# Kernel tuning notes

Measured on AMD Instinct MI355X. Metric: run time of the kernel, lower is better.

The kernel has to match this reference:

```python
import jax, jax.numpy as jnp
import numpy as np

B, T, L = 256, 2048, 48  # batch, seq_len, nb_labels


def setup_inputs() -> dict:
    key = jax.random.key(0)
    k1, k2, k3 = jax.random.split(key, 3)
    emissions = jax.random.normal(k1, (B, T, L), dtype=jnp.float32)
    tags = jax.random.randint(k2, (B, T), 0, L, dtype=jnp.int32)
    # matches nn.init.uniform_(transitions, -0.1, 0.1)
    transitions = jax.random.uniform(k3, (L, L), dtype=jnp.float32, minval=-0.1, maxval=0.1)
    return {"emissions": emissions, "tags": tags, "transitions": transitions}


def _gold_scores(emissions, tags, transitions):
    # emission score at every gold tag: [B, T] -> sum over T
    e = jnp.take_along_axis(emissions, tags[..., None], axis=2)[..., 0].sum(axis=1)
    # transition scores between consecutive gold tags
    t = transitions[tags[:, :-1], tags[:, 1:]].sum(axis=1)
    start = transitions[0, tags[:, 0]]      # row 0 acts as start scores
    end = transitions[tags[:, -1], -1]      # last column acts as end scores
    return e + t + start + end              # [B]


def _log_partition(emissions, transitions):
    # forward algorithm: alpha_t[b, j] = logsumexp_i(alpha_{t-1}[b, i] + T[i, j]) + em[b, t, j]
    alpha0 = transitions[0][None, :] + emissions[:, 0]          # [B, L]
    em_rest = jnp.moveaxis(emissions[:, 1:], 1, 0)              # [T-1, B, L]

    def step(alpha, em_t):
        alpha = jax.nn.logsumexp(alpha[:, :, None] + transitions[None, :, :], axis=1) + em_t
        return alpha, None

    alpha, _ = jax.lax.scan(step, alpha0, em_rest)
    return jax.nn.logsumexp(alpha + transitions[:, -1][None, :], axis=1)  # [B]


def reference(emissions, tags, transitions):
    """neg_log_likelihood of LinearChainCRF: -sum(scores - log_partition)."""
    scores = _gold_scores(emissions, tags, transitions)
    partition = _log_partition(emissions, transitions)
    return -jnp.sum(scores - partition)
```

## Files before the change

### kernel.cpp

```cpp
#include <hip/hip_runtime.h>

#define B 256
#define T 2048
#define L 48
#define G 16
#define SEG 128
#define KNORM 4.371f
#define TOTALF (B * T * L)

typedef short v4s __attribute__((ext_vector_type(4)));
typedef short v8s __attribute__((ext_vector_type(8)));
typedef float v4f __attribute__((ext_vector_type(4)));
typedef int   v2i __attribute__((ext_vector_type(2)));

#define WAVE_SYNC() asm volatile("s_waitcnt lgkmcnt(0)" ::: "memory")

#if __has_builtin(__builtin_amdgcn_mfma_f32_16x16x16bf16_1k)
#define MFMA16(a, b, c) __builtin_amdgcn_mfma_f32_16x16x16bf16_1k((a), (b), (c), 0, 0, 0)
#else
__device__ __forceinline__ v4f mfma16_asm(v4s a, v4s b, v4f c) {
    asm volatile("v_mfma_f32_16x16x16_bf16 %0, %1, %2, %0\n\ts_nop 7\n\ts_nop 7"
                 : "+v"(c) : "v"(a), "v"(b));
    return c;
}
#define MFMA16(a, b, c) mfma16_asm((a), (b), (c))
#endif

#if __has_builtin(__builtin_amdgcn_mfma_f32_16x16x32_bf16)
typedef __bf16 v8y __attribute__((ext_vector_type(8)));
__device__ __forceinline__ v4f mfma32(v8s a, v8s b, v4f c) {
    return __builtin_amdgcn_mfma_f32_16x16x32_bf16(
        __builtin_bit_cast(v8y, a), __builtin_bit_cast(v8y, b), c, 0, 0, 0);
}
#else
__device__ __forceinline__ v4f mfma32(v8s a, v8s b, v4f c) {
    asm volatile("v_mfma_f32_16x16x32_bf16 %0, %1, %2, %0\n\ts_nop 7\n\ts_nop 7"
                 : "+v"(c) : "v"(a), "v"(b));
    return c;
}
#endif

__device__ __forceinline__ unsigned cvt_pk(float lo, float hi) {
    unsigned r;
    asm("v_cvt_pk_bf16_f32 %0, %1, %2" : "=v"(r) : "v"(lo), "v"(hi));
    return r;
}

__device__ __forceinline__ v4s scale_pack2(v4f ca, v4f cb, v4f g) {
    v4f a = (ca + cb) * g;
    v2i d;
    d.x = (int)cvt_pk(a.x, a.y);
    d.y = (int)cvt_pk(a.z, a.w);
    return __builtin_bit_cast(v4s, d);
}

__device__ __forceinline__ v8s fuse01(v4s n0, v4s n1) {
    v2i a_ = __builtin_bit_cast(v2i, n0);
    v2i b_ = __builtin_bit_cast(v2i, n1);
    int4 fw; fw.x = a_.x; fw.y = a_.y; fw.z = b_.x; fw.w = b_.y;
    return __builtin_bit_cast(v8s, fw);
}

__global__ __launch_bounds__(192, 6) void crf_scan(
    const float* __restrict__ em, const int* __restrict__ tags,
    const float* __restrict__ trans, float* __restrict__ out,
    float* __restrict__ ws)
{
    const int b   = blockIdx.x >> 4;
    const int s   = blockIdx.x & 15;
    const int tid = threadIdx.x;
    const int ct  = tid >> 6;
    const int ln  = tid & 63;
    const int q   = ln >> 4;
    const int c   = ln & 15;

    __shared__ __align__(16) float smem[2 * 384];

    const size_t bem = (size_t)b * T * L;
    const int t0 = 1 + SEG * s;
    const int t1 = (t0 + SEG < T) ? (t0 + SEG) : T;

    v8s A32[3];
    #pragma unroll
    for (int rt = 0; rt < 3; ++rt) {
        const int m = 16 * rt + c;
        uint4 aw;
        aw.x = cvt_pk(__expf(trans[(4 * q + 0) * L + m]),
                      __expf(trans[(4 * q + 1) * L + m]));
        aw.y = cvt_pk(__expf(trans[(4 * q + 2) * L + m]),
                      __expf(trans[(4 * q + 3) * L + m]));
        aw.z = cvt_pk(__expf(trans[(16 + 4 * q + 0) * L + m]),
                      __expf(trans[(16 + 4 * q + 1) * L + m]));
        aw.w = cvt_pk(__expf(trans[(16 + 4 * q + 2) * L + m]),
                      __expf(trans[(16 + 4 * q + 3) * L + m]));
        A32[rt] = __builtin_bit_cast(v8s, aw);
    }
    v4s A16[3];
    #pragma unroll
    for (int rt = 0; rt < 3; ++rt) {
        const int m = 16 * rt + c;
        v2i d;
        d.x = (int)cvt_pk(__expf(trans[(32 + 4 * q + 0) * L + m]),
                          __expf(trans[(32 + 4 * q + 1) * L + m]));
        d.y = (int)cvt_pk(__expf(trans[(32 + 4 * q + 2) * L + m]),
                          __expf(trans[(32 + 4 * q + 3) * L + m]));
        A16[rt] = __builtin_bit_cast(v4s, d);
    }

    const int col = 16 * ct + c;
    v8s Bq01;
    v4s Bq2;
    {
        int4 w;
        w.x = (4 * q + 0 == col ? 0x3F80 : 0) | (4 * q + 1 == col ? 0x3F800000 : 0);
        w.y = (4 * q + 2 == col ? 0x3F80 : 0) | (4 * q + 3 == col ? 0x3F800000 : 0);
        w.z = (16 + 4 * q + 0 == col ? 0x3F80 : 0) | (16 + 4 * q + 1 == col ? 0x3F800000 : 0);
        w.w = (16 + 4 * q + 2 == col ? 0x3F80 : 0) | (16 + 4 * q + 3 == col ? 0x3F800000 : 0);
        Bq01 = __builtin_bit_cast(v8s, w);
        v2i d2;
        d2.x = (32 + 4 * q + 0 == col ? 0x3F80 : 0) | (32 + 4 * q + 1 == col ? 0x3F800000 : 0);
        d2.y = (32 + 4 * q + 2 == col ? 0x3F80 : 0) | (32 + 4 * q + 3 == col ? 0x3F800000 : 0);
        Bq2 = __builtin_bit_cast(v4s, d2);
    }

    const v4f zero4 = {0.f, 0.f, 0.f, 0.f};

    auto do_step = [&](const float* rowp) {
        v4f gv0 = *(const v4f*)(rowp + 4 * q);
        v4f gv1 = *(const v4f*)(rowp + 16 + 4 * q);
        v4f gv2 = *(const v4f*)(rowp + 32 + 4 * q);
        v4f Ca0 = mfma32(A32[0], Bq01, zero4);
        v4f Ca1 = mfma32(A32[1], Bq01, zero4);
        v4f Ca2 = mfma32(A32[2], Bq01, zero4);
        v4f Cb0 = MFMA16(A16[0], Bq2, zero4);
        v4f Cb1 = MFMA16(A16[1], Bq2, zero4);
        v4f Cb2 = MFMA16(A16[2], Bq2, zero4);
        v4s n0 = scale_pack2(Ca0, Cb0, gv0);
        v4s n1 = scale_pack2(Ca1, Cb1, gv1);
        Bq2    = scale_pack2(Ca2, Cb2, gv2);
        Bq01   = fuse01(n0, n1);
    };

    {
        size_t gf = bem + (size_t)t0 * L;
        smem[tid]       = __expf(em[gf + tid]       - KNORM);
        smem[tid + 192] = __expf(em[gf + tid + 192] - KNORM);
        __syncthreads();
    }

    for (int bk = 0; bk < 16; ++bk) {
        const float* cur = smem + (bk & 1) * 384;
        float* nxt = smem + ((bk & 1) ^ 1) * 384;

        size_t gf = bem + (size_t)(t0 + 8 * (bk + 1)) * L;
        if (gf > (size_t)TOTALF - 384) gf = (size_t)TOTALF - 384;
        float stg0 = em[gf + tid];
        float stg1 = em[gf + tid + 192];

        #pragma unroll
        for (int k = 0; k < 8; ++k)
            if (t0 + 8 * bk + k < t1)
                do_step(cur + 48 * k);

        nxt[tid]       = __expf(stg0 - KNORM);
        nxt[tid + 192] = __expf(stg1 - KNORM);
        __syncthreads();
    }

    unsigned short* qs = (unsigned short*)ws + (size_t)(b * G + s) * 2304;
    v2i dt[3];
    {
        int4 w01 = __builtin_bit_cast(int4, Bq01);
        dt[0].x = w01.x; dt[0].y = w01.y;
        dt[1].x = w01.z; dt[1].y = w01.w;
        dt[2] = __builtin_bit_cast(v2i, Bq2);
    }
    #pragma unroll
    for (int kt = 0; kt < 3; ++kt) {
        v2i d = dt[kt];
        int r0 = 16 * kt + 4 * q;
        qs[(r0 + 0) * 48 + col] = (unsigned short)((unsigned)d.x & 0xffffu);
        qs[(r0 + 1) * 48 + col] = (unsigned short)((unsigned)d.x >> 16);
        qs[(r0 + 2) * 48 + col] = (unsigned short)((unsigned)d.y & 0xffffu);
        qs[(r0 + 3) * 48 + col] = (unsigned short)((unsigned)d.y >> 16);
    }

    const int* tg = tags + (size_t)b * T;
    float gp = 0.f;
    if (tid < 128) {
        int t = SEG * s + tid;
        int tag = tg[t];
        gp += em[bem + (size_t)t * L + tag];
        if (t < T - 1)  gp += trans[tag * L + tg[t + 1]];
        if (t == 0)     gp += trans[tag];
        if (t == T - 1) gp += trans[tag * L + (L - 1)];
    }
    #pragma unroll
    for (int off = 32; off; off >>= 1) gp += __shfl_xor(gp, off);
    __shared__ float red[3];
    if (ln == 0) red[ct] = gp;
    __syncthreads();
    if (tid == 0) atomicAdd(out, -(red[0] + red[1] + red[2]));
}

__global__ __launch_bounds__(64) void crf_combine(
    const float* __restrict__ em, const float* __restrict__ trans,
    const float* __restrict__ ws, float* __restrict__ out)
{
    const int b = blockIdx.x, l = threadIdx.x;
    const int lc = (l < L) ? l : (L - 1);

    __shared__ float us[64];

    const unsigned short* qb = (const unsigned short*)ws + (size_t)b * G * 2304;

    float u = (l < L) ? __expf(trans[l] + em[(size_t)b * T * L + l]) : 0.f;
    float logtot = 2047.0f * KNORM;

    uint4 pre[6];
    {
        const uint4* p = (const uint4*)(qb + lc * 48);
        #pragma unroll
        for (int ii = 0; ii < 6; ++ii) pre[ii] = p[ii];
    }

    for (int s = 0; s < G; ++s) {
        us[l] = u;
        uint4 cur[6];
        #pragma unroll
        for (int ii = 0; ii < 6; ++ii) cur[ii] = pre[ii];
        if (s + 1 < G) {
            const uint4* p = (const uint4*)(qb + (size_t)(s + 1) * 2304 + lc * 48);
            #pragma unroll
            for (int ii = 0; ii < 6; ++ii) pre[ii] = p[ii];
        }
        WAVE_SYNC();

        float acc = 0.f;
        #pragma unroll
        for (int ii = 0; ii < 6; ++ii) {
            unsigned w0 = cur[ii].x, w1 = cur[ii].y, w2 = cur[ii].z, w3 = cur[ii].w;
            int jj = ii * 8;
            acc = fmaf(__uint_as_float(w0 << 16),          us[jj + 0], acc);
            acc = fmaf(__uint_as_float(w0 & 0xffff0000u),  us[jj + 1], acc);
            acc = fmaf(__uint_as_float(w1 << 16),          us[jj + 2], acc);
            acc = fmaf(__uint_as_float(w1 & 0xffff0000u),  us[jj + 3], acc);
            acc = fmaf(__uint_as_float(w2 << 16),          us[jj + 4], acc);
            acc = fmaf(__uint_as_float(w2 & 0xffff0000u),  us[jj + 5], acc);
            acc = fmaf(__uint_as_float(w3 << 16),          us[jj + 6], acc);
            acc = fmaf(__uint_as_float(w3 & 0xffff0000u),  us[jj + 7], acc);
        }
        WAVE_SYNC();

        float r = __int_as_float(
            __builtin_amdgcn_readlane(__float_as_int(acc), 0));
        logtot += __logf(r);
        u = (l < L) ? acc * __builtin_amdgcn_rcpf(r) : 0.f;
    }

    float v = (l < L) ? u * __expf(trans[lc * L + (L - 1)]) : 0.f;
    #pragma unroll
    for (int off = 32; off; off >>= 1) v += __shfl_xor(v, off);
    if (l == 0) atomicAdd(out, logtot + __logf(v));
}

extern "C" void kernel_launch(void* const* d_in, const int* in_sizes, int n_in,
                              void* d_out, int out_size, void* d_ws, size_t ws_size,
                              hipStream_t stream) {
    const float* em    = (const float*)d_in[0];
    const int*   tags  = (const int*)  d_in[1];
    const float* trans = (const float*)d_in[2];
    float* out = (float*)d_out;
    float* ws  = (float*)d_ws;

    (void)hipMemsetAsync(out, 0, sizeof(float), stream);
    crf_scan   <<<B * G, 192, 0, stream>>>(em, tags, trans, out, ws);
    crf_combine<<<B,      64, 0, stream>>>(em, trans, ws, out);
}
```

Measured before the change: 284.5 us.

## Halve sequence segments per batch and chain MFMA accumulators

Splits each sequence into 8 segments of 256 steps instead of 16 of 128. This halves the number of blocks and the per-segment matrix products that the combine kernel must process, at the cost of a longer serial chain per block. It also chains the K=32 and K=16 MFMAs through a shared accumulator instead of summing two separate results, which removes vector adds but serialises the dependency between the two MFMAs. The gold-score loop is extended so it still covers 256 timesteps per segment.

```diff
diff --git a/kernel.cpp b/kernel.cpp
--- a/kernel.cpp
+++ b/kernel.cpp
@@ -3,8 +3,8 @@
 #define B 256
 #define T 2048
 #define L 48
-#define G 16
-#define SEG 128
+#define G 8
+#define SEG 256
 #define KNORM 4.371f
 #define TOTALF (B * T * L)
 
@@ -46,8 +46,8 @@
     return r;
 }
 
-__device__ __forceinline__ v4s scale_pack2(v4f ca, v4f cb, v4f g) {
-    v4f a = (ca + cb) * g;
+__device__ __forceinline__ v4s scale_pack(v4f cf, v4f g) {
+    v4f a = cf * g;
     v2i d;
     d.x = (int)cvt_pk(a.x, a.y);
     d.y = (int)cvt_pk(a.z, a.w);
@@ -66,8 +66,8 @@
     const float* __restrict__ trans, float* __restrict__ out,
     float* __restrict__ ws)
 {
-    const int b   = blockIdx.x >> 4;
-    const int s   = blockIdx.x & 15;
+    const int b   = blockIdx.x >> 3;
+    const int s   = blockIdx.x & 7;
     const int tid = threadIdx.x;
     const int ct  = tid >> 6;
     const int ln  = tid & 63;
@@ -129,16 +129,23 @@
         v4f gv0 = *(const v4f*)(rowp + 4 * q);
         v4f gv1 = *(const v4f*)(rowp + 16 + 4 * q);
         v4f gv2 = *(const v4f*)(rowp + 32 + 4 * q);
-        v4f Ca0 = mfma32(A32[0], Bq01, zero4);
-        v4f Ca1 = mfma32(A32[1], Bq01, zero4);
-        v4f Ca2 = mfma32(A32[2], Bq01, zero4);
-        v4f Cb0 = MFMA16(A16[0], Bq2, zero4);
-        v4f Cb1 = MFMA16(A16[1], Bq2, zero4);
-        v4f Cb2 = MFMA16(A16[2], Bq2, zero4);
-        v4s n0 = scale_pack2(Ca0, Cb0, gv0);
-        v4s n1 = scale_pack2(Ca1, Cb1, gv1);
-        Bq2    = scale_pack2(Ca2, Cb2, gv2);
-        Bq01   = fuse01(n0, n1);
+        v4f Cf0, Cf1, Cf2;
+        {
+            v4f acc = mfma32(A32[0], Bq01, zero4);
+            Cf0 = MFMA16(A16[0], Bq2, acc);
+        }
+        {
+            v4f acc = mfma32(A32[1], Bq01, zero4);
+            Cf1 = MFMA16(A16[1], Bq2, acc);
+        }
+        {
+            v4f acc = mfma32(A32[2], Bq01, zero4);
+            Cf2 = MFMA16(A16[2], Bq2, acc);
+        }
+        v4s n0 = scale_pack(Cf0, gv0);
+        v4s n1 = scale_pack(Cf1, gv1);
+        Bq01 = fuse01(n0, n1);
+        Bq2  = scale_pack(Cf2, gv2);
     };
 
     {
@@ -148,7 +155,7 @@
         __syncthreads();
     }
 
-    for (int bk = 0; bk < 16; ++bk) {
+    for (int bk = 0; bk < SEG / 8; ++bk) {
         const float* cur = smem + (bk & 1) * 384;
         float* nxt = smem + ((bk & 1) ^ 1) * 384;
 
@@ -188,12 +195,15 @@
     const int* tg = tags + (size_t)b * T;
     float gp = 0.f;
     if (tid < 128) {
-        int t = SEG * s + tid;
-        int tag = tg[t];
-        gp += em[bem + (size_t)t * L + tag];
-        if (t < T - 1)  gp += trans[tag * L + tg[t + 1]];
-        if (t == 0)     gp += trans[tag];
-        if (t == T - 1) gp += trans[tag * L + (L - 1)];
+        #pragma unroll
+        for (int j = 0; j < 2; ++j) {
+            int t = SEG * s + 128 * j + tid;
+            int tag = tg[t];
+            gp += em[bem + (size_t)t * L + tag];
+            if (t < T - 1)  gp += trans[tag * L + tg[t + 1]];
+            if (t == 0)     gp += trans[tag];
+            if (t == T - 1) gp += trans[tag * L + (L - 1)];
+        }
     }
     #pragma unroll
     for (int off = 32; off; off >>= 1) gp += __shfl_xor(gp, off);
```

Measured after the change: 266.6 us. 6.3% less time.
